# Kernel optimization log

Hardware: AMD Instinct MI355X
Metric: run time of the kernel (lower is better)

## Reference

```python
import jax, jax.numpy as jnp
import numpy as np

N = 100_000          # nodes
E_RAND = 1_600_000   # random edges (avg degree 16)
IN, H, F, SEQ = 64, 4, 16, 10
FLAT = H * F * SEQ   # 640, MLP input width
MLP_DIMS = [FLAT, 180, 150, 128, 80, 64, 32, 1]


def setup_inputs() -> dict:
    key = jax.random.key(0)
    ks = jax.random.split(key, 32)
    x = jax.random.normal(ks[0], (N, IN), jnp.float32)
    # edges + self loops (dgl.add_self_loop)
    src = jnp.concatenate([jax.random.randint(ks[1], (E_RAND,), 0, N), jnp.arange(N)]).astype(jnp.int32)
    dst = jnp.concatenate([jax.random.randint(ks[2], (E_RAND,), 0, N), jnp.arange(N)]).astype(jnp.int32)
    inp = {"x": x, "src": src, "dst": dst}
    # GATConv params (fc has no bias in DGL; bias added post-aggregation)
    inp["fc_w"] = (jax.random.normal(ks[3], (IN, H * F), jnp.float32) / np.sqrt(IN).astype(np.float32))
    inp["bias"] = jnp.zeros((H * F,), jnp.float32)
    inp["attn_l"] = jax.random.normal(ks[4], (H, F), jnp.float32) * 0.1
    inp["attn_r"] = jax.random.normal(ks[5], (H, F), jnp.float32) * 0.1
    # deep MLP params
    for i in range(7):
        di, do = MLP_DIMS[i], MLP_DIMS[i + 1]
        inp[f"w{i+1}"] = jax.random.normal(ks[6 + i], (di, do), jnp.float32) / np.sqrt(di).astype(np.float32)
        inp[f"b{i+1}"] = jnp.zeros((do,), jnp.float32)
    inp["wt"] = jax.random.normal(ks[20], (FLAT, 1), jnp.float32) / np.sqrt(FLAT).astype(np.float32)
    return inp


def reference(x, src, dst, fc_w, bias, attn_l, attn_r,
              w1, b1, w2, b2, w3, b3, w4, b4, w5, b5, w6, b6, w7, b7, wt):
    # --- GATConv ---
    feat = (x @ fc_w).reshape(N, H, F)                      # [N,H,F]
    el = jnp.einsum('nhf,hf->nh', feat, attn_l)             # [N,H]
    er = jnp.einsum('nhf,hf->nh', feat, attn_r)
    e = jax.nn.leaky_relu(el[src] + er[dst], 0.2)           # [E,H]
    # edge softmax over incoming edges of each dst node
    m = jax.ops.segment_max(e, dst, num_segments=N)         # [N,H]
    ez = jnp.exp(e - m[dst])
    denom = jax.ops.segment_sum(ez, dst, num_segments=N)
    alpha = ez / denom[dst]                                 # [E,H]
    msg = alpha[:, :, None] * feat[src]                     # [E,H,F]
    out = jax.ops.segment_sum(msg, dst, num_segments=N) + bias.reshape(1, H, F)
    # --- flatten SEQ nodes per path, deep MLP + linear_trans ---
    g = out.reshape(N // SEQ, FLAT)                         # [P,640]
    h = g
    layers = [(w1, b1), (w2, b2), (w3, b3), (w4, b4), (w5, b5), (w6, b6), (w7, b7)]
    for i, (w, b) in enumerate(layers):
        h = h @ w + b
        if i < len(layers) - 1:
            h = jax.nn.relu(h)
    wx = g @ wt                                             # [P,1]
    return h + wx
```

## Files before the change

kernel.cpp:

```cpp
#include <hip/hip_runtime.h>
#include <hip/hip_bf16.h>
#include <hip/hip_fp16.h>

#define N_NODES 100000
#define P_PATHS 10000
#define NBUK 391
#define FEAT_BLKS 391
#define HIST_BLKS 416
#define WPREP_BLKS 94

typedef __attribute__((ext_vector_type(8))) short s16x8;
typedef __attribute__((ext_vector_type(4))) short s16x4;
typedef __attribute__((ext_vector_type(4))) float f32x4;
typedef __attribute__((ext_vector_type(8))) _Float16 f16x8;

__device__ __forceinline__ short f2bf(float v) {
    return __builtin_bit_cast(short, __float2bfloat16(v));
}
__device__ __forceinline__ float bf2f(short s) {
    return __bfloat162float(__builtin_bit_cast(__hip_bfloat16, s));
}
__device__ __forceinline__ float h2f(short s) {
    return __half2float(__builtin_bit_cast(__half, s));
}
__device__ __forceinline__ short f2h(float v) {
    return __builtin_bit_cast(short, __float2half(v));
}

__global__ __launch_bounds__(256) void k_fused1(const float* __restrict__ x,
                                                const float* __restrict__ fc_w,
                                                const float* __restrict__ attn_l,
                                                const float* __restrict__ attn_r,
                                                __half* __restrict__ feat,
                                                float* __restrict__ el,
                                                float* __restrict__ er,
                                                const int* __restrict__ dst,
                                                int* __restrict__ buktot,
                                                const float* __restrict__ w1,
                                                const float* __restrict__ w2,
                                                const float* __restrict__ w3,
                                                const float* __restrict__ w4,
                                                const float* __restrict__ w5,
                                                const float* __restrict__ w6,
                                                short* __restrict__ wf, int E) {
    __shared__ float s_w[64 * 64];
    __shared__ float s_wx[64 * 16];
    __shared__ int hcnt[NBUK];
    int tid = threadIdx.x;
    int bb = blockIdx.x;

    if (bb < FEAT_BLKS) {
        for (int i = tid; i < 4096; i += 256) s_w[i] = fc_w[i];
        __syncthreads();
        for (int i = tid; i < 1024; i += 256) {
            int k = i >> 4, c = i & 15;
            float v = 0.f;
            if (c < 8) {
                int h = c & 3;
                const float* av = (c < 4) ? attn_l : attn_r;
                for (int f = 0; f < 16; ++f) v += s_w[k * 64 + h * 16 + f] * av[h * 16 + f];
            }
            s_wx[i] = v;
        }
        __syncthreads();

        int w = tid >> 6, l = tid & 63;
        int c_lane = l & 15, kg = l >> 4;

        s16x8 wh[5][2], wlo[5][2];
#pragma unroll
        for (int ct = 0; ct < 5; ++ct)
#pragma unroll
            for (int ks = 0; ks < 2; ++ks) {
                s16x8 h8, l8;
#pragma unroll
                for (int i = 0; i < 8; ++i) {
                    int k = ks * 32 + kg * 8 + i;
                    float v = (ct < 4) ? s_w[k * 64 + ct * 16 + c_lane]
                                       : s_wx[k * 16 + c_lane];
                    short hi = f2bf(v);
                    h8[i] = hi;
                    l8[i] = f2bf(v - bf2f(hi));
                }
                wh[ct][ks] = h8;
                wlo[ct][ks] = l8;
            }

        int nbase = bb * 256 + w * 64;
#pragma unroll 1
        for (int mt = 0; mt < 4; ++mt) {
            int m0 = nbase + mt * 16;
            if (m0 >= N_NODES) break;
            int arow = m0 + c_lane;
            size_t axoff = (size_t)(arow < N_NODES ? arow : N_NODES - 1) * 64;
            s16x8 ah[2], alo[2];
#pragma unroll
            for (int ks = 0; ks < 2; ++ks) {
                const float* xp = x + axoff + ks * 32 + kg * 8;
                float4 v0 = *(const float4*)xp;
                float4 v1 = *(const float4*)(xp + 4);
                float vv[8] = {v0.x, v0.y, v0.z, v0.w, v1.x, v1.y, v1.z, v1.w};
                s16x8 h8, l8;
#pragma unroll
                for (int i = 0; i < 8; ++i) {
                    short hi = f2bf(vv[i]);
                    h8[i] = hi;
                    l8[i] = f2bf(vv[i] - bf2f(hi));
                }
                ah[ks] = h8;
                alo[ks] = l8;
            }
            int r0 = m0 + kg * 4;
#pragma unroll
            for (int ct = 0; ct < 5; ++ct) {
                f32x4 acc = {0.f, 0.f, 0.f, 0.f};
#pragma unroll
                for (int ks = 0; ks < 2; ++ks) {
                    acc = __builtin_amdgcn_mfma_f32_16x16x32_bf16(ah[ks], wh[ct][ks], acc, 0, 0, 0);
                    acc = __builtin_amdgcn_mfma_f32_16x16x32_bf16(ah[ks], wlo[ct][ks], acc, 0, 0, 0);
                    acc = __builtin_amdgcn_mfma_f32_16x16x32_bf16(alo[ks], wh[ct][ks], acc, 0, 0, 0);
                }
                if (ct < 4) {
#pragma unroll
                    for (int j = 0; j < 4; ++j) {
                        int r = r0 + j;
                        if (r < N_NODES)
                            feat[(size_t)r * 64 + ct * 16 + c_lane] = __float2half(acc[j]);
                    }
                } else {
                    if (c_lane < 4) {
#pragma unroll
                        for (int j = 0; j < 4; ++j) {
                            int r = r0 + j;
                            if (r < N_NODES) el[r * 4 + c_lane] = acc[j];
                        }
                    } else if (c_lane < 8) {
#pragma unroll
                        for (int j = 0; j < 4; ++j) {
                            int r = r0 + j;
                            if (r < N_NODES) er[r * 4 + (c_lane - 4)] = acc[j];
                        }
                    }
                }
            }
        }
    } else if (bb < FEAT_BLKS + HIST_BLKS) {
        int hb = bb - FEAT_BLKS;
        for (int i = tid; i < NBUK; i += 256) hcnt[i] = 0;
        __syncthreads();
#pragma unroll
        for (int j = 0; j < 4; ++j) {
            int i = hb * 4096 + j * 1024 + tid * 4;
            if (i + 3 < E) {
                int4 d4 = *(const int4*)(dst + i);
                atomicAdd(&hcnt[d4.x >> 8], 1);
                atomicAdd(&hcnt[d4.y >> 8], 1);
                atomicAdd(&hcnt[d4.z >> 8], 1);
                atomicAdd(&hcnt[d4.w >> 8], 1);
            } else {
                for (int k = i; k < E && k < i + 4; ++k)
                    atomicAdd(&hcnt[dst[k] >> 8], 1);
            }
        }
        __syncthreads();
        for (int i = tid; i < NBUK; i += 256)
            if (hcnt[i]) atomicAdd(buktot + i, hcnt[i]);
    } else {
        const int nblk[6] = {240, 60, 40, 20, 12, 4};
        const int din_[6] = {640, 180, 150, 128, 80, 64};
        const int dout_[6] = {180, 150, 128, 80, 64, 32};
        const int ks_[6]  = {20, 6, 5, 4, 3, 2};
        const int off_[6] = {0, 122880, 153600, 174080, 184320, 190464};
        const float* wp[6] = {w1, w2, w3, w4, w5, w6};

        int b = (bb - FEAT_BLKS - HIST_BLKS) * 4 + (tid >> 6);
        int layer = 0;
        while (layer < 5 && b >= nblk[layer]) { b -= nblk[layer]; ++layer; }
        int KS = ks_[layer];
        int ct = b / KS, ks = b % KS;
        int l = tid & 63;
        int c = ct * 16 + (l & 15);
        int k0 = ks * 32 + ((l >> 4) * 8);
        int din = din_[layer], dout = dout_[layer];
        const float* w = wp[layer];
        s16x8 vh;
#pragma unroll
        for (int i = 0; i < 8; ++i) {
            int k = k0 + i;
            float v = (k < din && c < dout) ? w[k * dout + c] : 0.f;
            vh[i] = f2h(v);
        }
        size_t o = (size_t)off_[layer] + ((size_t)(ct * KS + ks) * 64 + l) * 8;
        *(s16x8*)(wf + o) = vh;
    }
}

__global__ __launch_bounds__(512) void k_scanB(const int* __restrict__ buktot,
                                               int* __restrict__ bukstart,
                                               int* __restrict__ bukptr,
                                               int* __restrict__ rowptr, int E) {
    __shared__ int s[512];
    int tid = threadIdx.x;
    int v = (tid < NBUK) ? buktot[tid] : 0;
    s[tid] = v;
    __syncthreads();
    for (int off = 1; off < 512; off <<= 1) {
        int t = (tid >= off) ? s[tid - off] : 0;
        __syncthreads();
        s[tid] += t;
        __syncthreads();
    }
    int excl = s[tid] - v;
    if (tid < NBUK) { bukstart[tid] = excl; bukptr[tid] = excl; }
    if (tid == 0) { bukstart[NBUK] = E; rowptr[N_NODES] = E; }
}

__global__ __launch_bounds__(256) void k_bucketA(const int* __restrict__ src,
                                                 const int* __restrict__ dst,
                                                 int* __restrict__ bukptr,
                                                 uint2* __restrict__ pair, int E) {
    __shared__ int cnt[NBUK];
    __shared__ int base[NBUK];
    int tid = threadIdx.x;
    for (int i = tid; i < NBUK; i += 256) cnt[i] = 0;
    __syncthreads();
    int b0 = blockIdx.x * 2048;
    int s[8], d[8], off[8];
#pragma unroll
    for (int j = 0; j < 8; ++j) {
        int i = b0 + j * 256 + tid;
        if (i < E) {
            s[j] = src[i];
            d[j] = dst[i];
            off[j] = atomicAdd(&cnt[d[j] >> 8], 1);
        } else {
            d[j] = -1; s[j] = 0; off[j] = 0;
        }
    }
    __syncthreads();
    for (int i = tid; i < NBUK; i += 256)
        base[i] = cnt[i] ? atomicAdd(bukptr + i, cnt[i]) : 0;
    __syncthreads();
#pragma unroll
    for (int j = 0; j < 8; ++j) {
        if (d[j] >= 0) {
            int pos = base[d[j] >> 8] + off[j];
            pair[pos] = make_uint2((unsigned)s[j], (unsigned)d[j]);
        }
    }
}

__global__ __launch_bounds__(256) void k_bucketC(const uint2* __restrict__ pair,
                                                 const int* __restrict__ bukstart,
                                                 int* __restrict__ rowptr,
                                                 int* __restrict__ csr, int E) {
    __shared__ int cnt[256];
    __shared__ int s[256];
    __shared__ int wofs[256];
    int buk = blockIdx.x, tid = threadIdx.x;
    int p0 = bukstart[buk], p1 = bukstart[buk + 1];
    cnt[tid] = 0;
    __syncthreads();
    for (int i = p0 + tid; i < p1; i += 256)
        atomicAdd(&cnt[pair[i].y & 255], 1);
    __syncthreads();
    int v = cnt[tid];
    s[tid] = v;
    __syncthreads();
    for (int off = 1; off < 256; off <<= 1) {
        int t = (tid >= off) ? s[tid - off] : 0;
        __syncthreads();
        s[tid] += t;
        __syncthreads();
    }
    int r = p0 + s[tid] - v;
    wofs[tid] = r;
    int node = (buk << 8) + tid;
    if (node < N_NODES) rowptr[node] = r;
    __syncthreads();
    for (int i = p0 + tid; i < p1; i += 256) {
        uint2 p = pair[i];
        int pos = atomicAdd(&wofs[(int)p.y & 255], 1);
        csr[pos] = (int)p.x;
    }
}

__global__ __launch_bounds__(256) void k_agg(const int* __restrict__ rowptr,
                                             const int* __restrict__ csr,
                                             const float* __restrict__ el,
                                             const float* __restrict__ er,
                                             const __half* __restrict__ feat,
                                             const float* __restrict__ bias,
                                             float* __restrict__ agg) {
    int tid = threadIdx.x;
    int wave = tid >> 6, lane = tid & 63;
    int slot = lane >> 4;
    int fl = lane & 15;
    int n = blockIdx.x * 4 + wave;
    if (n >= N_NODES) return;
    int h = fl >> 2;
    float ern = er[(size_t)n * 4 + h];
    int e0 = rowptr[n], e1 = rowptr[n + 1];
    f32x4 a0 = {0.f, 0.f, 0.f, 0.f}, a1 = {0.f, 0.f, 0.f, 0.f};
    float den0 = 0.f, den1 = 0.f;
    int e = e0 + slot;
    for (; e + 4 < e1; e += 8) {
        int s0 = csr[e], s1 = csr[e + 4];
        s16x4 v0 = *(const s16x4*)(feat + (size_t)s0 * 64 + fl * 4);
        s16x4 v1 = *(const s16x4*)(feat + (size_t)s1 * 64 + fl * 4);
        float ev0 = el[(size_t)s0 * 4 + h] + ern;
        float ev1 = el[(size_t)s1 * 4 + h] + ern;
        ev0 = ev0 > 0.f ? ev0 : 0.2f * ev0;
        ev1 = ev1 > 0.f ? ev1 : 0.2f * ev1;
        float ez0 = __expf(ev0);
        float ez1 = __expf(ev1);
#pragma unroll
        for (int t = 0; t < 4; ++t) {
            a0[t] += ez0 * h2f(v0[t]);
            a1[t] += ez1 * h2f(v1[t]);
        }
        den0 += ez0;
        den1 += ez1;
    }
    for (; e < e1; e += 4) {
        int s0 = csr[e];
        s16x4 v0 = *(const s16x4*)(feat + (size_t)s0 * 64 + fl * 4);
        float ev0 = el[(size_t)s0 * 4 + h] + ern;
        ev0 = ev0 > 0.f ? ev0 : 0.2f * ev0;
        float ez0 = __expf(ev0);
#pragma unroll
        for (int t = 0; t < 4; ++t)
            a0[t] += ez0 * h2f(v0[t]);
        den0 += ez0;
    }
    f32x4 a;
    float den = den0 + den1;
#pragma unroll
    for (int t = 0; t < 4; ++t) a[t] = a0[t] + a1[t];
#pragma unroll
    for (int t = 0; t < 4; ++t) {
        a[t] += __shfl_xor(a[t], 32);
        a[t] += __shfl_xor(a[t], 16);
    }
    den += __shfl_xor(den, 32);
    den += __shfl_xor(den, 16);
    if (slot == 0) {
        float4 o;
        float inv = 1.f / den;
        o.x = a[0] * inv + bias[fl * 4 + 0];
        o.y = a[1] * inv + bias[fl * 4 + 1];
        o.z = a[2] * inv + bias[fl * 4 + 2];
        o.w = a[3] * inv + bias[fl * 4 + 3];
        *(float4*)(agg + (size_t)n * 64 + fl * 4) = o;
    }
}

template <int KS, int CT>
__device__ __forceinline__ void mfma_layer16(const short* sa, int sstride,
                                             short* dst_,
                                             const short* __restrict__ wf,
                                             const float* __restrict__ bias,
                                             int dout, int w, int l) {
    int abase = (l & 15) * sstride + ((l >> 4) * 8);
    int c_lane = l & 15;
    for (int ct = w; ct < CT; ct += 4) {
        f32x4 acc = {0.f, 0.f, 0.f, 0.f};
        const f16x8* wp = (const f16x8*)wf + (size_t)(ct * KS) * 64 + l;
#pragma unroll
        for (int ks = 0; ks < KS; ++ks) {
            f16x8 av = *(const f16x8*)(sa + abase + ks * 32);
            f16x8 wv = wp[ks * 64];
            acc = __builtin_amdgcn_mfma_f32_16x16x32_f16(av, wv, acc, 0, 0, 0);
        }
        int c = ct * 16 + c_lane;
        float bb = (c < dout) ? bias[c] : 0.f;
        int row0 = (l >> 4) * 4;
#pragma unroll
        for (int j = 0; j < 4; ++j) {
            float v = acc[j] + bb;
            v = v > 0.f ? v : 0.f;
            dst_[(row0 + j) * 200 + c] = f2h(v);
        }
    }
}

__global__ __launch_bounds__(256) void k_mlp(const float* __restrict__ agg,
                                             const short* __restrict__ wf,
                                             const float* __restrict__ b1,
                                             const float* __restrict__ b2,
                                             const float* __restrict__ b3,
                                             const float* __restrict__ b4,
                                             const float* __restrict__ b5,
                                             const float* __restrict__ b6,
                                             const float* __restrict__ w7,
                                             const float* __restrict__ b7,
                                             const float* __restrict__ wt,
                                             float* __restrict__ outp) {
    __shared__ __align__(16) short smem[13600];
    __shared__ float wx[16];
    short* g  = smem;
    short* h0 = smem + 10368;
    short* h1 = smem;

    int tid = threadIdx.x;
    int w = tid >> 6, l = tid & 63;
    int p0 = blockIdx.x * 16;

    const float4* a4 = (const float4*)(agg + (size_t)p0 * 640);
    for (int i = tid; i < 16 * 160; i += 256) {
        int r = i / 160, c4 = (i % 160) * 4;
        float4 v = a4[i];
        s16x4 hv;
        hv[0] = f2h(v.x); hv[1] = f2h(v.y); hv[2] = f2h(v.z); hv[3] = f2h(v.w);
        *(s16x4*)(g + r * 648 + c4) = hv;
    }

    if (tid < 128) {
        int path = tid >> 3, sub = tid & 7;
        const float* gr = agg + (size_t)(p0 + path) * 640;
        float acc = 0.f;
        for (int k = sub * 4; k < 640; k += 32) {
            float4 gv = *(const float4*)(gr + k);
            float4 wv = *(const float4*)(wt + k);
            acc += gv.x * wv.x + gv.y * wv.y + gv.z * wv.z + gv.w * wv.w;
        }
        acc += __shfl_xor(acc, 1);
        acc += __shfl_xor(acc, 2);
        acc += __shfl_xor(acc, 4);
        if (sub == 0) wx[path] = acc;
    }
    __syncthreads();

    mfma_layer16<20, 12>(g, 648, h0, wf + 0,      b1, 180, w, l);
    __syncthreads();
    mfma_layer16<6, 10>(h0, 200, h1, wf + 122880, b2, 150, w, l);
    __syncthreads();
    mfma_layer16<5, 8>(h1, 200, h0, wf + 153600, b3, 128, w, l);
    __syncthreads();
    mfma_layer16<4, 5>(h0, 200, h1, wf + 174080, b4, 80, w, l);
    {
        int r = tid >> 4, c = 80 + (tid & 15);
        h1[r * 200 + c] = 0;
    }
    __syncthreads();
    mfma_layer16<3, 4>(h1, 200, h0, wf + 184320, b5, 64, w, l);
    __syncthreads();
    mfma_layer16<2, 2>(h0, 200, h1, wf + 190464, b6, 32, w, l);
    __syncthreads();

    if (tid < 16) {
        float acc = b7[0];
#pragma unroll
        for (int k = 0; k < 32; ++k)
            acc += h2f(h1[tid * 200 + k]) * w7[k];
        outp[p0 + tid] = acc + wx[tid];
    }
}

extern "C" void kernel_launch(void* const* d_in, const int* in_sizes, int n_in,
                              void* d_out, int out_size, void* d_ws, size_t ws_size,
                              hipStream_t stream) {
    const float* x      = (const float*)d_in[0];
    const int*   src    = (const int*)d_in[1];
    const int*   dst    = (const int*)d_in[2];
    const float* fc_w   = (const float*)d_in[3];
    const float* bias   = (const float*)d_in[4];
    const float* attn_l = (const float*)d_in[5];
    const float* attn_r = (const float*)d_in[6];
    const float* w1 = (const float*)d_in[7];  const float* b1 = (const float*)d_in[8];
    const float* w2 = (const float*)d_in[9];  const float* b2 = (const float*)d_in[10];
    const float* w3 = (const float*)d_in[11]; const float* b3 = (const float*)d_in[12];
    const float* w4 = (const float*)d_in[13]; const float* b4 = (const float*)d_in[14];
    const float* w5 = (const float*)d_in[15]; const float* b5 = (const float*)d_in[16];
    const float* w6 = (const float*)d_in[17]; const float* b6 = (const float*)d_in[18];
    const float* w7 = (const float*)d_in[19]; const float* b7 = (const float*)d_in[20];
    const float* wt = (const float*)d_in[21];
    int E = in_sizes[1];

    float* ws      = (float*)d_ws;
    __half* feat   = (__half*)ws;
    float* el      = ws + 6400000;
    float* er      = ws + 6800000;
    float* agg     = ws + 7200000;
    uint2* pair    = (uint2*)(ws + 7200000);
    int*   rowptr  = (int*)(ws + 13600000);
    int*   buktot  = (int*)(ws + 13700004);
    int*   bukstart= (int*)(ws + 13700400);
    int*   bukptr  = (int*)(ws + 13700800);
    int*   csr     = (int*)(ws + 13701200);
    short* wf      = (short*)(ws + 13701200 + E);

    int nwgA = (E + 2047) / 2048;

    hipMemsetAsync(buktot, 0, NBUK * 4, stream);

    k_fused1<<<FEAT_BLKS + HIST_BLKS + WPREP_BLKS, 256, 0, stream>>>(
        x, fc_w, attn_l, attn_r, feat, el, er, dst, buktot,
        w1, w2, w3, w4, w5, w6, wf, E);
    k_scanB<<<1, 512, 0, stream>>>(buktot, bukstart, bukptr, rowptr, E);
    k_bucketA<<<nwgA, 256, 0, stream>>>(src, dst, bukptr, pair, E);
    k_bucketC<<<NBUK, 256, 0, stream>>>(pair, bukstart, rowptr, csr, E);
    k_agg<<<N_NODES / 4, 256, 0, stream>>>(rowptr, csr, el, er, feat, bias, agg);
    k_mlp<<<P_PATHS / 16, 256, 0, stream>>>(agg, wf, b1, b2, b3, b4, b5, b6,
                                            w7, b7, wt, (float*)d_out);
}
```

Before: 178.1 us.

## Pack bucket pairs into 32-bit words and store aggregated features as fp16

The bucket sort intermediate now packs the source index (17 bits) and the low 8 bits of the destination into one 32-bit word instead of a uint2, halving that scratch traffic. The GAT aggregation output is written as fp16 rather than fp32, so the MLP kernel loads half the bytes and copies them straight into shared memory without converting. The wx linear term now reads fp16 inputs, adding a small rounding step it did not have before, though the MLP path already rounded to fp16. Packing assumes node ids below 2^17 and moves the pair buffer to its own workspace region.

```diff
diff --git a/kernel.cpp b/kernel.cpp
--- a/kernel.cpp
+++ b/kernel.cpp
@@ -218,7 +218,7 @@
 __global__ __launch_bounds__(256) void k_bucketA(const int* __restrict__ src,
                                                  const int* __restrict__ dst,
                                                  int* __restrict__ bukptr,
-                                                 uint2* __restrict__ pair, int E) {
+                                                 unsigned* __restrict__ pair, int E) {
     __shared__ int cnt[NBUK];
     __shared__ int base[NBUK];
     int tid = threadIdx.x;
@@ -245,12 +245,12 @@
     for (int j = 0; j < 8; ++j) {
         if (d[j] >= 0) {
             int pos = base[d[j] >> 8] + off[j];
-            pair[pos] = make_uint2((unsigned)s[j], (unsigned)d[j]);
-        }
-    }
-}
-
-__global__ __launch_bounds__(256) void k_bucketC(const uint2* __restrict__ pair,
+            pair[pos] = (unsigned)s[j] | ((unsigned)(d[j] & 255) << 17);
+        }
+    }
+}
+
+__global__ __launch_bounds__(256) void k_bucketC(const unsigned* __restrict__ pair,
                                                  const int* __restrict__ bukstart,
                                                  int* __restrict__ rowptr,
                                                  int* __restrict__ csr, int E) {
@@ -262,7 +262,7 @@
     cnt[tid] = 0;
     __syncthreads();
     for (int i = p0 + tid; i < p1; i += 256)
-        atomicAdd(&cnt[pair[i].y & 255], 1);
+        atomicAdd(&cnt[pair[i] >> 17], 1);
     __syncthreads();
     int v = cnt[tid];
     s[tid] = v;
@@ -279,9 +279,9 @@
     if (node < N_NODES) rowptr[node] = r;
     __syncthreads();
     for (int i = p0 + tid; i < p1; i += 256) {
-        uint2 p = pair[i];
-        int pos = atomicAdd(&wofs[(int)p.y & 255], 1);
-        csr[pos] = (int)p.x;
+        unsigned p = pair[i];
+        int pos = atomicAdd(&wofs[p >> 17], 1);
+        csr[pos] = (int)(p & 0x1FFFFu);
     }
 }
 
@@ -291,7 +291,7 @@
                                              const float* __restrict__ er,
                                              const __half* __restrict__ feat,
                                              const float* __restrict__ bias,
-                                             float* __restrict__ agg) {
+                                             __half* __restrict__ agg) {
     int tid = threadIdx.x;
     int wave = tid >> 6, lane = tid & 63;
     int slot = lane >> 4;
@@ -345,13 +345,13 @@
     den += __shfl_xor(den, 32);
     den += __shfl_xor(den, 16);
     if (slot == 0) {
-        float4 o;
         float inv = 1.f / den;
-        o.x = a[0] * inv + bias[fl * 4 + 0];
-        o.y = a[1] * inv + bias[fl * 4 + 1];
-        o.z = a[2] * inv + bias[fl * 4 + 2];
-        o.w = a[3] * inv + bias[fl * 4 + 3];
-        *(float4*)(agg + (size_t)n * 64 + fl * 4) = o;
+        s16x4 o;
+        o[0] = f2h(a[0] * inv + bias[fl * 4 + 0]);
+        o[1] = f2h(a[1] * inv + bias[fl * 4 + 1]);
+        o[2] = f2h(a[2] * inv + bias[fl * 4 + 2]);
+        o[3] = f2h(a[3] * inv + bias[fl * 4 + 3]);
+        *(s16x4*)(agg + (size_t)n * 64 + fl * 4) = o;
     }
 }
 
@@ -384,7 +384,7 @@
     }
 }
 
-__global__ __launch_bounds__(256) void k_mlp(const float* __restrict__ agg,
+__global__ __launch_bounds__(256) void k_mlp(const __half* __restrict__ agg,
                                              const short* __restrict__ wf,
                                              const float* __restrict__ b1,
                                              const float* __restrict__ b2,
@@ -406,23 +406,21 @@
     int w = tid >> 6, l = tid & 63;
     int p0 = blockIdx.x * 16;
 
-    const float4* a4 = (const float4*)(agg + (size_t)p0 * 640);
-    for (int i = tid; i < 16 * 160; i += 256) {
-        int r = i / 160, c4 = (i % 160) * 4;
-        float4 v = a4[i];
-        s16x4 hv;
-        hv[0] = f2h(v.x); hv[1] = f2h(v.y); hv[2] = f2h(v.z); hv[3] = f2h(v.w);
-        *(s16x4*)(g + r * 648 + c4) = hv;
+    const s16x8* a8 = (const s16x8*)(agg + (size_t)p0 * 640);
+    for (int i = tid; i < 16 * 80; i += 256) {
+        int r = i / 80, c8 = (i % 80) * 8;
+        *(s16x8*)(g + r * 648 + c8) = a8[i];
     }
 
     if (tid < 128) {
         int path = tid >> 3, sub = tid & 7;
-        const float* gr = agg + (size_t)(p0 + path) * 640;
+        const __half* gr = agg + (size_t)(p0 + path) * 640;
         float acc = 0.f;
         for (int k = sub * 4; k < 640; k += 32) {
-            float4 gv = *(const float4*)(gr + k);
+            s16x4 gv = *(const s16x4*)(gr + k);
             float4 wv = *(const float4*)(wt + k);
-            acc += gv.x * wv.x + gv.y * wv.y + gv.z * wv.z + gv.w * wv.w;
+            acc += h2f(gv[0]) * wv.x + h2f(gv[1]) * wv.y
+                 + h2f(gv[2]) * wv.z + h2f(gv[3]) * wv.w;
         }
         acc += __shfl_xor(acc, 1);
         acc += __shfl_xor(acc, 2);
@@ -481,8 +479,8 @@
     __half* feat   = (__half*)ws;
     float* el      = ws + 6400000;
     float* er      = ws + 6800000;
-    float* agg     = ws + 7200000;
-    uint2* pair    = (uint2*)(ws + 7200000);
+    __half* agg    = (__half*)(ws + 7200000);
+    unsigned* pair = (unsigned*)(ws + 10400000);
     int*   rowptr  = (int*)(ws + 13600000);
     int*   buktot  = (int*)(ws + 13700004);
     int*   bukstart= (int*)(ws + 13700400);
```

Result: faster. 168.3 us (-5.5%).
